# Optimization experiments

Hardware: AMD Instinct MI355X
Metric: run time of the kernel (lower is better)

Reference implementation:

```python
import jax, jax.numpy as jnp
import numpy as np

H = 1024      # hidden_size
L = 2         # decoder_layers
V = 50257     # output_size (vocab)
S = 2048      # encoder seq_len (max_length)


def gru_cell(x, h, W_ih, W_hh, b_ih, b_hh):
    # x: [1, in], h: [1, H]; PyTorch GRU gate order: r, z, n
    gi = x @ W_ih.T + b_ih          # [1, 3H]
    gh = h @ W_hh.T + b_hh          # [1, 3H]
    i_r, i_z, i_n = jnp.split(gi, 3, axis=1)
    h_r, h_z, h_n = jnp.split(gh, 3, axis=1)
    r = jax.nn.sigmoid(i_r + h_r)
    z = jax.nn.sigmoid(i_z + h_z)
    n = jnp.tanh(i_n + r * h_n)
    return (1.0 - z) * n + z * h


def setup_inputs() -> dict:
    key = jax.random.key(0)
    ks = jax.random.split(key, 12)
    w = 0.02  # weight scale to keep activations sane
    return {
        "word_input": jax.random.randint(ks[0], (1,), 0, V, dtype=jnp.int64)
            if jax.config.jax_enable_x64 else jax.random.randint(ks[0], (1,), 0, V),
        "last_context": jax.random.normal(ks[1], (1, H), jnp.float32),
        "last_hidden": jax.random.normal(ks[2], (L, 1, H), jnp.float32),
        "encoder_outputs": jax.random.normal(ks[3], (S, 1, H), jnp.float32),
        "emb": jax.random.normal(ks[4], (V, H), jnp.float32) * w,
        "W_ih0": jax.random.normal(ks[5], (3 * H, 2 * H), jnp.float32) * w,
        "W_hh0": jax.random.normal(ks[6], (3 * H, H), jnp.float32) * w,
        "b_ih0": jnp.zeros((3 * H,), jnp.float32),
        "b_hh0": jnp.zeros((3 * H,), jnp.float32),
        "W_ih1": jax.random.normal(ks[7], (3 * H, H), jnp.float32) * w,
        "W_hh1": jax.random.normal(ks[8], (3 * H, H), jnp.float32) * w,
        "b_ih1": jnp.zeros((3 * H,), jnp.float32),
        "b_hh1": jnp.zeros((3 * H,), jnp.float32),
        "W_out": jax.random.normal(ks[9], (V, 2 * H), jnp.float32) * w,
        "b_out": jnp.zeros((V,), jnp.float32),
    }


def reference(word_input, last_context, last_hidden, encoder_outputs, emb,
              W_ih0, W_hh0, b_ih0, b_hh0, W_ih1, W_hh1, b_ih1, b_hh1,
              W_out, b_out):
    # embedding + concat with previous context -> GRU step input [1, 2H]
    word_embedded = emb[word_input]                       # [1, H]
    rnn_input = jnp.concatenate([word_embedded, last_context], axis=1)

    h0 = gru_cell(rnn_input, last_hidden[0], W_ih0, W_hh0, b_ih0, b_hh0)
    h1 = gru_cell(h0, last_hidden[1], W_ih1, W_hh1, b_ih1, b_hh1)
    hidden = jnp.stack([h0, h1], axis=0)                  # [L, 1, H]
    rnn_output = h1                                       # [1, H]

    # Attn 'general' in the source discards the Linear and uses a plain dot:
    enc = encoder_outputs[:, 0, :]                        # [S, H]
    energies = enc @ rnn_output[0]                        # [S]
    attn_weights = jax.nn.softmax(energies)[None, None, :]  # [1, 1, S]
    context = attn_weights[0] @ enc                       # [1, H]

    logits = jnp.concatenate([rnn_output, context], axis=1) @ W_out.T + b_out
    output = jax.nn.log_softmax(logits, axis=1)           # [1, V]
    return (output, context, hidden, attn_weights)
```

## Files before the change

kernel.cpp:

```cpp
#include <hip/hip_runtime.h>

#define H 1024
#define SEQ 2048
#define V 50257

#define OUT_CTX   50257
#define OUT_H0    (OUT_CTX + H)
#define OUT_H1    (OUT_H0 + H)
#define OUT_ATTN  (OUT_H1 + H)

#define WS_X      0
#define WS_H0     2048
#define WS_H1     3072
#define WS_E      4096
#define WS_ATTN   6144
#define WS_CTX    8192
#define WS_LOGITS 9216
#define WS_PM     59473
#define WS_PS     59601
#define WS_LOGZ   59729

__device__ __forceinline__ float dot4(float4 a, float4 b) {
  return a.x * b.x + a.y * b.y + a.z * b.z + a.w * b.w;
}

__device__ __forceinline__ float wave_reduce_sum(float v) {
  #pragma unroll
  for (int off = 32; off > 0; off >>= 1) v += __shfl_down(v, off);
  return v;
}

__global__ __launch_bounds__(256) void prep_kernel(
    const float* __restrict__ emb, const int* __restrict__ word,
    const float* __restrict__ last_context,
    float* __restrict__ rnn_input, float* __restrict__ ctx_acc) {
  int i = blockIdx.x * 256 + threadIdx.x;
  int w = word[0];
  rnn_input[i]     = emb[(size_t)w * H + i];
  rnn_input[H + i] = last_context[i];
  ctx_acc[i] = 0.0f;
}

template <int XDIM>
__global__ __launch_bounds__(384) void gru_kernel(
    const float* __restrict__ x,
    const float* __restrict__ hprev,
    const float* __restrict__ W_ih,
    const float* __restrict__ W_hh,
    const float* __restrict__ b_ih,
    const float* __restrict__ b_hh,
    float* __restrict__ h_ws, float* __restrict__ h_out) {
  int j = blockIdx.x;
  int wave = threadIdx.x >> 6, lane = threadIdx.x & 63;
  __shared__ float parts[6];
  float acc = 0.0f;
  if (wave < 3) {
    const float4* wr = (const float4*)(W_ih + (size_t)(wave * H + j) * XDIM);
    const float4* xv = (const float4*)x;
    #pragma unroll
    for (int it = 0; it < XDIM / 256; ++it) {
      int idx = it * 64 + lane;
      acc += dot4(wr[idx], xv[idx]);
    }
  } else {
    const float4* wr = (const float4*)(W_hh + (size_t)((wave - 3) * H + j) * H);
    const float4* hv = (const float4*)hprev;
    #pragma unroll
    for (int it = 0; it < H / 256; ++it) {
      int idx = it * 64 + lane;
      acc += dot4(wr[idx], hv[idx]);
    }
  }
  acc = wave_reduce_sum(acc);
  if (lane == 0) parts[wave] = acc;
  __syncthreads();
  if (threadIdx.x == 0) {
    float gi_r = parts[0] + b_ih[j];
    float gi_z = parts[1] + b_ih[H + j];
    float gi_n = parts[2] + b_ih[2 * H + j];
    float gh_r = parts[3] + b_hh[j];
    float gh_z = parts[4] + b_hh[H + j];
    float gh_n = parts[5] + b_hh[2 * H + j];
    float r = 1.0f / (1.0f + expf(-(gi_r + gh_r)));
    float z = 1.0f / (1.0f + expf(-(gi_z + gh_z)));
    float n = tanhf(gi_n + r * gh_n);
    float hp = hprev[j];
    float hn = (1.0f - z) * n + z * hp;
    h_ws[j] = hn;
    h_out[j] = hn;
  }
}

__global__ __launch_bounds__(256) void energies_kernel(
    const float* __restrict__ enc, const float* __restrict__ h1,
    float* __restrict__ energies) {
  int s = blockIdx.x * 4 + (threadIdx.x >> 6);
  int lane = threadIdx.x & 63;
  const float4* er = (const float4*)(enc + (size_t)s * H);
  const float4* hv = (const float4*)h1;
  float acc = 0.0f;
  #pragma unroll
  for (int it = 0; it < H / 256; ++it) {
    int idx = it * 64 + lane;
    acc += dot4(er[idx], hv[idx]);
  }
  acc = wave_reduce_sum(acc);
  if (lane == 0) energies[s] = acc;
}

__global__ __launch_bounds__(1024) void softmax_kernel(
    const float* __restrict__ energies, float* __restrict__ attn_ws,
    float* __restrict__ attn_out) {
  __shared__ float red[1024];
  int t = threadIdx.x;
  float e0 = energies[t], e1 = energies[t + 1024];
  red[t] = fmaxf(e0, e1);
  __syncthreads();
  #pragma unroll
  for (int off = 512; off > 0; off >>= 1) {
    if (t < off) red[t] = fmaxf(red[t], red[t + off]);
    __syncthreads();
  }
  float M = red[0];
  __syncthreads();
  float s0 = expf(e0 - M), s1 = expf(e1 - M);
  red[t] = s0 + s1;
  __syncthreads();
  #pragma unroll
  for (int off = 512; off > 0; off >>= 1) {
    if (t < off) red[t] += red[t + off];
    __syncthreads();
  }
  float Z = red[0];
  float a0 = s0 / Z, a1 = s1 / Z;
  attn_ws[t] = a0;
  attn_ws[t + 1024] = a1;
  attn_out[t] = a0;
  attn_out[t + 1024] = a1;
}

__global__ __launch_bounds__(256) void context_kernel(
    const float* __restrict__ attn, const float* __restrict__ enc,
    float* __restrict__ ctx) {
  int h2 = blockIdx.x * 512 + threadIdx.x * 2;
  int s0 = blockIdx.y * 32;
  float a0 = 0.0f, a1 = 0.0f;
  for (int s = s0; s < s0 + 32; ++s) {
    float a = attn[s];
    float2 p = *(const float2*)(enc + (size_t)s * H + h2);
    a0 += a * p.x;
    a1 += a * p.y;
  }
  atomicAdd(&ctx[h2], a0);
  atomicAdd(&ctx[h2 + 1], a1);
}

__global__ __launch_bounds__(256) void logits_kernel(
    const float* __restrict__ W_out, const float* __restrict__ b_out,
    const float* __restrict__ h1, const float* __restrict__ ctx,
    float* __restrict__ logits) {
  __shared__ float y[2 * H];
  int t = threadIdx.x;
  #pragma unroll
  for (int i = 0; i < 4; ++i) { int k = t + i * 256; y[k] = h1[k]; }
  #pragma unroll
  for (int i = 0; i < 4; ++i) { int k = t + i * 256; y[H + k] = ctx[k]; }
  __syncthreads();
  int v = blockIdx.x * 4 + (t >> 6);
  if (v >= V) return;
  int lane = t & 63;
  const float4* wr = (const float4*)(W_out + (size_t)v * (2 * H));
  const float4* yv = (const float4*)y;
  float acc = 0.0f;
  #pragma unroll
  for (int it = 0; it < (2 * H) / 256; ++it) {
    int idx = it * 64 + lane;
    acc += dot4(wr[idx], yv[idx]);
  }
  acc = wave_reduce_sum(acc);
  if (lane == 0) logits[v] = acc + b_out[v];
}

__global__ __launch_bounds__(256) void reduce_kernel(
    const float* __restrict__ logits, float* __restrict__ pm, float* __restrict__ ps) {
  __shared__ float red[256];
  int t = threadIdx.x;
  int i0 = blockIdx.x * 256 + t;
  int i1 = i0 + 32768;
  float v0 = (i0 < V) ? logits[i0] : -INFINITY;
  float v1 = (i1 < V) ? logits[i1] : -INFINITY;
  red[t] = fmaxf(v0, v1);
  __syncthreads();
  #pragma unroll
  for (int off = 128; off > 0; off >>= 1) {
    if (t < off) red[t] = fmaxf(red[t], red[t + off]);
    __syncthreads();
  }
  float M = red[0];
  __syncthreads();
  float s = 0.0f;
  if (i0 < V) s += expf(v0 - M);
  if (i1 < V) s += expf(v1 - M);
  red[t] = s;
  __syncthreads();
  #pragma unroll
  for (int off = 128; off > 0; off >>= 1) {
    if (t < off) red[t] += red[t + off];
    __syncthreads();
  }
  if (t == 0) { pm[blockIdx.x] = M; ps[blockIdx.x] = red[0]; }
}

__global__ __launch_bounds__(128) void lse_final_kernel(
    const float* __restrict__ pm, const float* __restrict__ ps, float* __restrict__ logZ) {
  __shared__ float red[128];
  int t = threadIdx.x;
  float m = pm[t];
  red[t] = m;
  __syncthreads();
  #pragma unroll
  for (int off = 64; off > 0; off >>= 1) {
    if (t < off) red[t] = fmaxf(red[t], red[t + off]);
    __syncthreads();
  }
  float M = red[0];
  __syncthreads();
  red[t] = ps[t] * expf(m - M);
  __syncthreads();
  #pragma unroll
  for (int off = 64; off > 0; off >>= 1) {
    if (t < off) red[t] += red[t + off];
    __syncthreads();
  }
  if (t == 0) logZ[0] = M + logf(red[0]);
}

__global__ __launch_bounds__(256) void finalize_kernel(
    const float* __restrict__ logits, const float* __restrict__ logZ,
    const float* __restrict__ ctx, float* __restrict__ out) {
  int v = blockIdx.x * 256 + threadIdx.x;
  float lz = logZ[0];
  if (v < V) out[v] = logits[v] - lz;
  if (v < H) out[OUT_CTX + v] = ctx[v];
}

extern "C" void kernel_launch(void* const* d_in, const int* in_sizes, int n_in,
                              void* d_out, int out_size, void* d_ws, size_t ws_size,
                              hipStream_t stream) {
  const int*   word         = (const int*)d_in[0];
  const float* last_context = (const float*)d_in[1];
  const float* last_hidden  = (const float*)d_in[2];
  const float* enc          = (const float*)d_in[3];
  const float* emb          = (const float*)d_in[4];
  const float* W_ih0        = (const float*)d_in[5];
  const float* W_hh0        = (const float*)d_in[6];
  const float* b_ih0        = (const float*)d_in[7];
  const float* b_hh0        = (const float*)d_in[8];
  const float* W_ih1        = (const float*)d_in[9];
  const float* W_hh1        = (const float*)d_in[10];
  const float* b_ih1        = (const float*)d_in[11];
  const float* b_hh1        = (const float*)d_in[12];
  const float* W_out        = (const float*)d_in[13];
  const float* b_out        = (const float*)d_in[14];
  float* out = (float*)d_out;

  float* ws       = (float*)d_ws;
  float* rnn_in   = ws + WS_X;
  float* h0       = ws + WS_H0;
  float* h1       = ws + WS_H1;
  float* energies = ws + WS_E;
  float* attn     = ws + WS_ATTN;
  float* ctx      = ws + WS_CTX;
  float* logits   = ws + WS_LOGITS;
  float* pm       = ws + WS_PM;
  float* ps       = ws + WS_PS;
  float* logZ     = ws + WS_LOGZ;

  prep_kernel<<<4, 256, 0, stream>>>(emb, word, last_context, rnn_in, ctx);
  gru_kernel<2 * H><<<H, 384, 0, stream>>>(rnn_in, last_hidden, W_ih0, W_hh0,
                                           b_ih0, b_hh0, h0, out + OUT_H0);
  gru_kernel<H><<<H, 384, 0, stream>>>(h0, last_hidden + H, W_ih1, W_hh1,
                                       b_ih1, b_hh1, h1, out + OUT_H1);
  energies_kernel<<<SEQ / 4, 256, 0, stream>>>(enc, h1, energies);
  softmax_kernel<<<1, 1024, 0, stream>>>(energies, attn, out + OUT_ATTN);
  context_kernel<<<dim3(2, 64), 256, 0, stream>>>(attn, enc, ctx);
  logits_kernel<<<(V + 3) / 4, 256, 0, stream>>>(W_out, b_out, h1, ctx, logits);
  reduce_kernel<<<128, 256, 0, stream>>>(logits, pm, ps);
  lse_final_kernel<<<1, 128, 0, stream>>>(pm, ps, logZ);
  finalize_kernel<<<(V + 255) / 256, 256, 0, stream>>>(logits, logZ, ctx, out);
}
```

Baseline: 693.8 us.

## Fuse prep, softmax and logsumexp partials into neighbouring kernels

Folds the embedding/concat prep into the first GRU kernel and computes per-block max/sum partials for the attention softmax inside the energies kernel. The context kernel then normalises its own attention slice, so the separate softmax kernel goes away. The logits kernel handles 50 rows per block with two rows in flight per wave and keeps a running logsumexp, which removes the separate reduce kernel. The aim is to cut launch count and extra global passes, at the cost of a redundant reduction of the softmax partials in every context block and more work per logits block.

```diff
diff --git a/kernel.cpp b/kernel.cpp
--- a/kernel.cpp
+++ b/kernel.cpp
@@ -1,4 +1,5 @@
 #include <hip/hip_runtime.h>
+#include <float.h>
 
 #define H 1024
 #define SEQ 2048
@@ -9,69 +10,62 @@
 #define OUT_H1    (OUT_H0 + H)
 #define OUT_ATTN  (OUT_H1 + H)
 
-#define WS_X      0
-#define WS_H0     2048
-#define WS_H1     3072
-#define WS_E      4096
-#define WS_ATTN   6144
-#define WS_CTX    8192
-#define WS_LOGITS 9216
-#define WS_PM     59473
-#define WS_PS     59601
-#define WS_LOGZ   59729
+#define WS_H0     0
+#define WS_H1     1024
+#define WS_E      2048
+#define WS_EPM    4096
+#define WS_EPS    4608
+#define WS_CTX    5120
+#define WS_LOGITS 6144
+#define WS_LPM    56448
+#define WS_LPS    57472
+#define WS_LOGZ   58496
+
+#define LOGITS_ROWS_PB 50
+#define LOGITS_NB      ((V + LOGITS_ROWS_PB - 1) / LOGITS_ROWS_PB)
 
 __device__ __forceinline__ float dot4(float4 a, float4 b) {
   return a.x * b.x + a.y * b.y + a.z * b.z + a.w * b.w;
 }
 
-__device__ __forceinline__ float wave_reduce_sum(float v) {
-  #pragma unroll
-  for (int off = 32; off > 0; off >>= 1) v += __shfl_down(v, off);
+__device__ __forceinline__ float wave_allreduce_sum(float v) {
+  #pragma unroll
+  for (int off = 32; off > 0; off >>= 1) v += __shfl_xor(v, off);
   return v;
 }
 
-__global__ __launch_bounds__(256) void prep_kernel(
+__global__ __launch_bounds__(384) void gru0_kernel(
     const float* __restrict__ emb, const int* __restrict__ word,
     const float* __restrict__ last_context,
-    float* __restrict__ rnn_input, float* __restrict__ ctx_acc) {
-  int i = blockIdx.x * 256 + threadIdx.x;
-  int w = word[0];
-  rnn_input[i]     = emb[(size_t)w * H + i];
-  rnn_input[H + i] = last_context[i];
-  ctx_acc[i] = 0.0f;
-}
-
-template <int XDIM>
-__global__ __launch_bounds__(384) void gru_kernel(
-    const float* __restrict__ x,
     const float* __restrict__ hprev,
     const float* __restrict__ W_ih,
     const float* __restrict__ W_hh,
-    const float* __restrict__ b_ih,
-    const float* __restrict__ b_hh,
+    const float* __restrict__ b_ih, const float* __restrict__ b_hh,
     float* __restrict__ h_ws, float* __restrict__ h_out) {
   int j = blockIdx.x;
   int wave = threadIdx.x >> 6, lane = threadIdx.x & 63;
   __shared__ float parts[6];
   float acc = 0.0f;
   if (wave < 3) {
-    const float4* wr = (const float4*)(W_ih + (size_t)(wave * H + j) * XDIM);
-    const float4* xv = (const float4*)x;
-    #pragma unroll
-    for (int it = 0; it < XDIM / 256; ++it) {
+    const float4* wr = (const float4*)(W_ih + (size_t)(wave * H + j) * (2 * H));
+    const float4* e4 = (const float4*)(emb + (size_t)word[0] * H);
+    const float4* c4 = (const float4*)last_context;
+    #pragma unroll
+    for (int it = 0; it < 8; ++it) {
       int idx = it * 64 + lane;
-      acc += dot4(wr[idx], xv[idx]);
+      float4 xv = (it < 4) ? e4[idx] : c4[idx - 256];
+      acc += dot4(wr[idx], xv);
     }
   } else {
     const float4* wr = (const float4*)(W_hh + (size_t)((wave - 3) * H + j) * H);
     const float4* hv = (const float4*)hprev;
     #pragma unroll
-    for (int it = 0; it < H / 256; ++it) {
+    for (int it = 0; it < 4; ++it) {
       int idx = it * 64 + lane;
       acc += dot4(wr[idx], hv[idx]);
     }
   }
-  acc = wave_reduce_sum(acc);
+  acc = wave_allreduce_sum(acc);
   if (lane == 0) parts[wave] = acc;
   __syncthreads();
   if (threadIdx.x == 0) {
@@ -91,105 +85,198 @@
   }
 }
 
+__global__ __launch_bounds__(384) void gru1_kernel(
+    const float* __restrict__ x,
+    const float* __restrict__ hprev,
+    const float* __restrict__ W_ih,
+    const float* __restrict__ W_hh,
+    const float* __restrict__ b_ih, const float* __restrict__ b_hh,
+    float* __restrict__ h_ws, float* __restrict__ h_out) {
+  int j = blockIdx.x;
+  int wave = threadIdx.x >> 6, lane = threadIdx.x & 63;
+  __shared__ float parts[6];
+  const float* W   = (wave < 3) ? W_ih : W_hh;
+  const float* vec = (wave < 3) ? x : hprev;
+  int row = (wave < 3) ? wave : (wave - 3);
+  const float4* wr = (const float4*)(W + (size_t)(row * H + j) * H);
+  const float4* xv = (const float4*)vec;
+  float acc = 0.0f;
+  #pragma unroll
+  for (int it = 0; it < 4; ++it) {
+    int idx = it * 64 + lane;
+    acc += dot4(wr[idx], xv[idx]);
+  }
+  acc = wave_allreduce_sum(acc);
+  if (lane == 0) parts[wave] = acc;
+  __syncthreads();
+  if (threadIdx.x == 0) {
+    float gi_r = parts[0] + b_ih[j];
+    float gi_z = parts[1] + b_ih[H + j];
+    float gi_n = parts[2] + b_ih[2 * H + j];
+    float gh_r = parts[3] + b_hh[j];
+    float gh_z = parts[4] + b_hh[H + j];
+    float gh_n = parts[5] + b_hh[2 * H + j];
+    float r = 1.0f / (1.0f + expf(-(gi_r + gh_r)));
+    float z = 1.0f / (1.0f + expf(-(gi_z + gh_z)));
+    float n = tanhf(gi_n + r * gh_n);
+    float hp = hprev[j];
+    float hn = (1.0f - z) * n + z * hp;
+    h_ws[j] = hn;
+    h_out[j] = hn;
+  }
+}
+
 __global__ __launch_bounds__(256) void energies_kernel(
     const float* __restrict__ enc, const float* __restrict__ h1,
-    float* __restrict__ energies) {
-  int s = blockIdx.x * 4 + (threadIdx.x >> 6);
-  int lane = threadIdx.x & 63;
+    float* __restrict__ energies, float* __restrict__ epm,
+    float* __restrict__ eps, float* __restrict__ ctx) {
+  int t = threadIdx.x;
+  if (blockIdx.x < 4) ctx[blockIdx.x * 256 + t] = 0.0f;
+  int wave = t >> 6, lane = t & 63;
+  int s = blockIdx.x * 4 + wave;
   const float4* er = (const float4*)(enc + (size_t)s * H);
   const float4* hv = (const float4*)h1;
   float acc = 0.0f;
   #pragma unroll
-  for (int it = 0; it < H / 256; ++it) {
+  for (int it = 0; it < 4; ++it) {
     int idx = it * 64 + lane;
     acc += dot4(er[idx], hv[idx]);
   }
-  acc = wave_reduce_sum(acc);
-  if (lane == 0) energies[s] = acc;
-}
-
-__global__ __launch_bounds__(1024) void softmax_kernel(
-    const float* __restrict__ energies, float* __restrict__ attn_ws,
-    float* __restrict__ attn_out) {
-  __shared__ float red[1024];
+  acc = wave_allreduce_sum(acc);
+  __shared__ float se[4];
+  if (lane == 0) { se[wave] = acc; energies[s] = acc; }
+  __syncthreads();
+  if (t == 0) {
+    float m = fmaxf(fmaxf(se[0], se[1]), fmaxf(se[2], se[3]));
+    float ss = expf(se[0] - m) + expf(se[1] - m) + expf(se[2] - m) + expf(se[3] - m);
+    epm[blockIdx.x] = m;
+    eps[blockIdx.x] = ss;
+  }
+}
+
+__global__ __launch_bounds__(256) void context_kernel(
+    const float* __restrict__ energies, const float* __restrict__ epm,
+    const float* __restrict__ eps, const float* __restrict__ enc,
+    float* __restrict__ ctx, float* __restrict__ attn_out) {
+  __shared__ float red[256];
+  __shared__ float satt[32];
   int t = threadIdx.x;
-  float e0 = energies[t], e1 = energies[t + 1024];
-  red[t] = fmaxf(e0, e1);
-  __syncthreads();
-  #pragma unroll
-  for (int off = 512; off > 0; off >>= 1) {
+  float m = fmaxf(epm[t], epm[t + 256]);
+  red[t] = m;
+  __syncthreads();
+  #pragma unroll
+  for (int off = 128; off > 0; off >>= 1) {
     if (t < off) red[t] = fmaxf(red[t], red[t + off]);
     __syncthreads();
   }
   float M = red[0];
   __syncthreads();
-  float s0 = expf(e0 - M), s1 = expf(e1 - M);
-  red[t] = s0 + s1;
-  __syncthreads();
-  #pragma unroll
-  for (int off = 512; off > 0; off >>= 1) {
+  red[t] = eps[t] * expf(epm[t] - M) + eps[t + 256] * expf(epm[t + 256] - M);
+  __syncthreads();
+  #pragma unroll
+  for (int off = 128; off > 0; off >>= 1) {
     if (t < off) red[t] += red[t + off];
     __syncthreads();
   }
-  float Z = red[0];
-  float a0 = s0 / Z, a1 = s1 / Z;
-  attn_ws[t] = a0;
-  attn_ws[t + 1024] = a1;
-  attn_out[t] = a0;
-  attn_out[t + 1024] = a1;
-}
-
-__global__ __launch_bounds__(256) void context_kernel(
-    const float* __restrict__ attn, const float* __restrict__ enc,
-    float* __restrict__ ctx) {
-  int h2 = blockIdx.x * 512 + threadIdx.x * 2;
+  float Zinv = 1.0f / red[0];
   int s0 = blockIdx.y * 32;
+  if (t < 32) satt[t] = expf(energies[s0 + t] - M) * Zinv;
+  __syncthreads();
+  int h2 = blockIdx.x * 512 + t * 2;
   float a0 = 0.0f, a1 = 0.0f;
-  for (int s = s0; s < s0 + 32; ++s) {
-    float a = attn[s];
-    float2 p = *(const float2*)(enc + (size_t)s * H + h2);
+  for (int i = 0; i < 32; ++i) {
+    float a = satt[i];
+    float2 p = *(const float2*)(enc + (size_t)(s0 + i) * H + h2);
     a0 += a * p.x;
     a1 += a * p.y;
   }
   atomicAdd(&ctx[h2], a0);
   atomicAdd(&ctx[h2 + 1], a1);
+  if (blockIdx.x == 0 && t < 32) attn_out[s0 + t] = satt[t];
 }
 
 __global__ __launch_bounds__(256) void logits_kernel(
     const float* __restrict__ W_out, const float* __restrict__ b_out,
     const float* __restrict__ h1, const float* __restrict__ ctx,
-    float* __restrict__ logits) {
+    float* __restrict__ logits, float* __restrict__ lpm,
+    float* __restrict__ lps) {
   __shared__ float y[2 * H];
+  __shared__ float wm[4], wsv[4];
   int t = threadIdx.x;
   #pragma unroll
-  for (int i = 0; i < 4; ++i) { int k = t + i * 256; y[k] = h1[k]; }
-  #pragma unroll
-  for (int i = 0; i < 4; ++i) { int k = t + i * 256; y[H + k] = ctx[k]; }
-  __syncthreads();
-  int v = blockIdx.x * 4 + (t >> 6);
-  if (v >= V) return;
-  int lane = t & 63;
-  const float4* wr = (const float4*)(W_out + (size_t)v * (2 * H));
+  for (int i = 0; i < 4; ++i) {
+    int k = t + i * 256;
+    y[k] = h1[k];
+    y[H + k] = ctx[k];
+  }
+  __syncthreads();
+  int wave = t >> 6, lane = t & 63;
   const float4* yv = (const float4*)y;
-  float acc = 0.0f;
-  #pragma unroll
-  for (int it = 0; it < (2 * H) / 256; ++it) {
-    int idx = it * 64 + lane;
-    acc += dot4(wr[idx], yv[idx]);
-  }
-  acc = wave_reduce_sum(acc);
-  if (lane == 0) logits[v] = acc + b_out[v];
-}
-
-__global__ __launch_bounds__(256) void reduce_kernel(
-    const float* __restrict__ logits, float* __restrict__ pm, float* __restrict__ ps) {
+  int base = blockIdx.x * LOGITS_ROWS_PB;
+  int rend = min(base + LOGITS_ROWS_PB, V);
+  float m = -FLT_MAX, s = 0.0f;
+  int r = base + wave;
+  for (; r + 4 < rend; r += 8) {
+    const float4* w0 = (const float4*)(W_out + (size_t)r * (2 * H));
+    const float4* w1 = (const float4*)(W_out + (size_t)(r + 4) * (2 * H));
+    float a0 = 0.0f, a1 = 0.0f;
+    #pragma unroll
+    for (int it = 0; it < 8; ++it) {
+      int idx = it * 64 + lane;
+      float4 yy = yv[idx];
+      a0 += dot4(w0[idx], yy);
+      a1 += dot4(w1[idx], yy);
+    }
+    #pragma unroll
+    for (int off = 32; off > 0; off >>= 1) {
+      a0 += __shfl_xor(a0, off);
+      a1 += __shfl_xor(a1, off);
+    }
+    float l0 = a0 + b_out[r];
+    float l1 = a1 + b_out[r + 4];
+    if (lane == 0) { logits[r] = l0; logits[r + 4] = l1; }
+    float nm = fmaxf(m, fmaxf(l0, l1));
+    s = s * expf(m - nm) + expf(l0 - nm) + expf(l1 - nm);
+    m = nm;
+  }
+  for (; r < rend; r += 4) {
+    const float4* w0 = (const float4*)(W_out + (size_t)r * (2 * H));
+    float a0 = 0.0f;
+    #pragma unroll
+    for (int it = 0; it < 8; ++it) {
+      int idx = it * 64 + lane;
+      a0 += dot4(w0[idx], yv[idx]);
+    }
+    a0 = wave_allreduce_sum(a0);
+    float l0 = a0 + b_out[r];
+    if (lane == 0) logits[r] = l0;
+    float nm = fmaxf(m, l0);
+    s = s * expf(m - nm) + expf(l0 - nm);
+    m = nm;
+  }
+  if (lane == 0) { wm[wave] = m; wsv[wave] = s; }
+  __syncthreads();
+  if (t == 0) {
+    float mb = fmaxf(fmaxf(wm[0], wm[1]), fmaxf(wm[2], wm[3]));
+    float sb = wsv[0] * expf(wm[0] - mb) + wsv[1] * expf(wm[1] - mb) +
+               wsv[2] * expf(wm[2] - mb) + wsv[3] * expf(wm[3] - mb);
+    lpm[blockIdx.x] = mb;
+    lps[blockIdx.x] = sb;
+  }
+}
+
+__global__ __launch_bounds__(256) void lse_final_kernel(
+    const float* __restrict__ lpm, const float* __restrict__ lps,
+    float* __restrict__ logZ) {
   __shared__ float red[256];
   int t = threadIdx.x;
-  int i0 = blockIdx.x * 256 + t;
-  int i1 = i0 + 32768;
-  float v0 = (i0 < V) ? logits[i0] : -INFINITY;
-  float v1 = (i1 < V) ? logits[i1] : -INFINITY;
-  red[t] = fmaxf(v0, v1);
+  float m = -FLT_MAX;
+  #pragma unroll
+  for (int i = 0; i < 4; ++i) {
+    int k = t + i * 256;
+    if (k < LOGITS_NB) m = fmaxf(m, lpm[k]);
+  }
+  red[t] = m;
   __syncthreads();
   #pragma unroll
   for (int off = 128; off > 0; off >>= 1) {
@@ -199,36 +286,15 @@
   float M = red[0];
   __syncthreads();
   float s = 0.0f;
-  if (i0 < V) s += expf(v0 - M);
-  if (i1 < V) s += expf(v1 - M);
+  #pragma unroll
+  for (int i = 0; i < 4; ++i) {
+    int k = t + i * 256;
+    if (k < LOGITS_NB) s += lps[k] * expf(lpm[k] - M);
+  }
   red[t] = s;
   __syncthreads();
   #pragma unroll
   for (int off = 128; off > 0; off >>= 1) {
-    if (t < off) red[t] += red[t + off];
-    __syncthreads();
-  }
-  if (t == 0) { pm[blockIdx.x] = M; ps[blockIdx.x] = red[0]; }
-}
-
-__global__ __launch_bounds__(128) void lse_final_kernel(
-    const float* __restrict__ pm, const float* __restrict__ ps, float* __restrict__ logZ) {
-  __shared__ float red[128];
-  int t = threadIdx.x;
-  float m = pm[t];
-  red[t] = m;
-  __syncthreads();
-  #pragma unroll
-  for (int off = 64; off > 0; off >>= 1) {
-    if (t < off) red[t] = fmaxf(red[t], red[t + off]);
-    __syncthreads();
-  }
-  float M = red[0];
-  __syncthreads();
-  red[t] = ps[t] * expf(m - M);
-  __syncthreads();
-  #pragma unroll
-  for (int off = 64; off > 0; off >>= 1) {
     if (t < off) red[t] += red[t + off];
     __syncthreads();
   }
@@ -265,27 +331,26 @@
   float* out = (float*)d_out;
 
   float* ws       = (float*)d_ws;
-  float* rnn_in   = ws + WS_X;
   float* h0       = ws + WS_H0;
   float* h1       = ws + WS_H1;
   float* energies = ws + WS_E;
-  float* attn     = ws + WS_ATTN;
+  float* epm      = ws + WS_EPM;
+  float* eps      = ws + WS_EPS;
   float* ctx      = ws + WS_CTX;
   float* logits   = ws + WS_LOGITS;
-  float* pm       = ws + WS_PM;
-  float* ps       = ws + WS_PS;
+  float* lpm      = ws + WS_LPM;
+  float* lps      = ws + WS_LPS;
   float* logZ     = ws + WS_LOGZ;
 
-  prep_kernel<<<4, 256, 0, stream>>>(emb, word, last_context, rnn_in, ctx);
-  gru_kernel<2 * H><<<H, 384, 0, stream>>>(rnn_in, last_hidden, W_ih0, W_hh0,
-                                           b_ih0, b_hh0, h0, out + OUT_H0);
-  gru_kernel<H><<<H, 384, 0, stream>>>(h0, last_hidden + H, W_ih1, W_hh1,
-                                       b_ih1, b_hh1, h1, out + OUT_H1);
-  energies_kernel<<<SEQ / 4, 256, 0, stream>>>(enc, h1, energies);
-  softmax_kernel<<<1, 1024, 0, stream>>>(energies, attn, out + OUT_ATTN);
-  context_kernel<<<dim3(2, 64), 256, 0, stream>>>(attn, enc, ctx);
-  logits_kernel<<<(V + 3) / 4, 256, 0, stream>>>(W_out, b_out, h1, ctx, logits);
-  reduce_kernel<<<128, 256, 0, stream>>>(logits, pm, ps);
-  lse_final_kernel<<<1, 128, 0, stream>>>(pm, ps, logZ);
+  gru0_kernel<<<H, 384, 0, stream>>>(emb, word, last_context, last_hidden,
+                                     W_ih0, W_hh0, b_ih0, b_hh0, h0, out + OUT_H0);
+  gru1_kernel<<<H, 384, 0, stream>>>(h0, last_hidden + H, W_ih1, W_hh1,
+                                     b_ih1, b_hh1, h1, out + OUT_H1);
+  energies_kernel<<<SEQ / 4, 256, 0, stream>>>(enc, h1, energies, epm, eps, ctx);
+  context_kernel<<<dim3(2, 64), 256, 0, stream>>>(energies, epm, eps, enc, ctx,
+                                                  out + OUT_ATTN);
+  logits_kernel<<<LOGITS_NB, 256, 0, stream>>>(W_out, b_out, h1, ctx, logits,
+                                               lpm, lps);
+  lse_final_kernel<<<1, 256, 0, stream>>>(lpm, lps, logZ);
   finalize_kernel<<<(V + 255) / 256, 256, 0, stream>>>(logits, logZ, ctx, out);
 }
```

Measured after the change: 691.2 us. Within noise of the previous version (-0.4%).
